# Kernel optimization log

Hardware: AMD Instinct MI355X
Metric: run time of the kernel (lower is better)

Reference implementation:

```python
import jax, jax.numpy as jnp
import numpy as np

D_MODEL = 1024
NUM_HEADS = 16
HEAD_DIM = D_MODEL // NUM_HEADS
B, S = 4, 2048


def setup_inputs() -> dict:
    key = jax.random.key(0)
    ks = jax.random.split(key, 12)
    s = 1.0 / np.sqrt(D_MODEL)
    return {
        "inputs_q": jax.random.normal(ks[0], (B, S, D_MODEL), jnp.float32),
        "inputs_k": jax.random.normal(ks[1], (B, S, D_MODEL), jnp.float32),
        "inputs_v": jax.random.normal(ks[2], (B, S, D_MODEL), jnp.float32),
        "Wq": jax.random.normal(ks[3], (D_MODEL, D_MODEL), jnp.float32) * s,
        "bq": jax.random.normal(ks[4], (D_MODEL,), jnp.float32) * 0.01,
        "Wk": jax.random.normal(ks[5], (D_MODEL, D_MODEL), jnp.float32) * s,
        "bk": jax.random.normal(ks[6], (D_MODEL,), jnp.float32) * 0.01,
        "Wv": jax.random.normal(ks[7], (D_MODEL, D_MODEL), jnp.float32) * s,
        "bv": jax.random.normal(ks[8], (D_MODEL,), jnp.float32) * 0.01,
        "Wo": jax.random.normal(ks[9], (D_MODEL, D_MODEL), jnp.float32) * s,
        "bo": jax.random.normal(ks[10], (D_MODEL,), jnp.float32) * 0.01,
    }


def reference(inputs_q, inputs_k, inputs_v, Wq, bq, Wk, bk, Wv, bv, Wo, bo):
    b, s, _ = inputs_q.shape
    # linear projections
    q = inputs_q @ Wq + bq  # [b, s, d_model]
    k = inputs_k @ Wk + bk
    v = inputs_v @ Wv + bv
    # split heads: bsd -> bhsd
    q = q.reshape(b, s, NUM_HEADS, HEAD_DIM).transpose(0, 2, 1, 3)
    k = k.reshape(b, s, NUM_HEADS, HEAD_DIM).transpose(0, 2, 1, 3)
    v = v.reshape(b, s, NUM_HEADS, HEAD_DIM).transpose(0, 2, 1, 3)
    scale = 1.0 / jnp.sqrt(jnp.asarray(HEAD_DIM, q.dtype))
    scores = jnp.einsum('bhqd,bhkd->bhqk', q, k) * scale  # [b,h,s,s]
    # causal mask: position q attends to k <= q
    causal = jnp.tril(jnp.ones((s, s), dtype=bool))
    scores = jnp.where(causal[None, None], scores, jnp.asarray(-jnp.inf, scores.dtype))
    attn = jax.nn.softmax(scores, axis=-1)
    ctx = jnp.einsum('bhqk,bhkd->bhqd', attn, v)  # [b,h,s,hd]
    ctx = ctx.transpose(0, 2, 1, 3).reshape(b, s, D_MODEL)
    return ctx @ Wo + bo
```

## Files before the change

### kernel.cpp

```cpp
#include <hip/hip_runtime.h>
#include <math.h>
#include <type_traits>

typedef __bf16 bf16;
typedef __attribute__((ext_vector_type(8))) __bf16 bf16x8;
typedef __attribute__((ext_vector_type(4))) float f32x4;

#define SEQ 2048
#define DM 1024
#define NH 16
#define HD 64
#define BATCH 4

#define NEG_BIG (-1e30f)
#define SCALE_L2E 0.18033688011f

__device__ inline bf16x8 cvt_f32x8(const float* p) {
  f32x4 x0 = *(const f32x4*)p;
  f32x4 x1 = *(const f32x4*)(p + 4);
  bf16x8 r;
  r[0] = (bf16)x0[0]; r[1] = (bf16)x0[1]; r[2] = (bf16)x0[2]; r[3] = (bf16)x0[3];
  r[4] = (bf16)x1[0]; r[5] = (bf16)x1[1]; r[6] = (bf16)x1[2]; r[7] = (bf16)x1[3];
  return r;
}

__device__ inline void async_copy16(const bf16* g, bf16* l) {
  __builtin_amdgcn_global_load_lds(
      (const __attribute__((address_space(1))) unsigned int*)g,
      (__attribute__((address_space(3))) unsigned int*)l, 16, 0, 0);
}

__global__ __launch_bounds__(256) void cvt_kernel(const float* __restrict__ src,
                                                  bf16* __restrict__ dst) {
  size_t i = ((size_t)blockIdx.x * 256 + threadIdx.x) * 8;
  *(bf16x8*)(dst + i) = cvt_f32x8(src + i);
}

__global__ __launch_bounds__(256) void transpose_w_kernel(
    const float* __restrict__ Wq, const float* __restrict__ Wk,
    const float* __restrict__ Wv, const float* __restrict__ Wo,
    bf16* __restrict__ Tq, bf16* __restrict__ Tk,
    bf16* __restrict__ Tv, bf16* __restrict__ To) {
  __shared__ bf16 tile[64 * 66];
  int z = blockIdx.z;
  const float* src = (z == 0) ? Wq : (z == 1) ? Wk : (z == 2) ? Wv : Wo;
  bf16* dst = (z == 0) ? Tq : (z == 1) ? Tk : (z == 2) ? Tv : To;
  int n0 = blockIdx.x * 64, k0 = blockIdx.y * 64;
  int t = threadIdx.x;
  int c = t & 63, rr = t >> 6;
#pragma unroll
  for (int i = 0; i < 16; i++) {
    int k = i * 4 + rr;
    tile[k * 66 + c] = (bf16)src[(size_t)(k0 + k) * DM + n0 + c];
  }
  __syncthreads();
#pragma unroll
  for (int i = 0; i < 16; i++) {
    int n = i * 4 + rr;
    dst[(size_t)(n0 + n) * DM + k0 + c] = tile[c * 66 + n];
  }
}

__global__ __launch_bounds__(256) void transpose_v_kernel(
    const bf16* __restrict__ Vc, bf16* __restrict__ Vt) {
  __shared__ bf16 tile[64 * 66];
  int s0 = blockIdx.x * 64;
  int bh = blockIdx.y;
  int t = threadIdx.x;
  int c = t & 63, rr = t >> 6;
  const bf16* src = Vc + (size_t)bh * SEQ * HD;
  bf16* dst = Vt + (size_t)bh * HD * SEQ;
#pragma unroll
  for (int i = 0; i < 16; i++) {
    int s = i * 4 + rr;
    tile[s * 66 + c] = src[(size_t)(s0 + s) * HD + c];
  }
  __syncthreads();
#pragma unroll
  for (int i = 0; i < 16; i++) {
    int d = i * 4 + rr;
    dst[(size_t)d * SEQ + s0 + c] = tile[c * 66 + d];
  }
}

template <typename CT, int MODE>
__global__ __launch_bounds__(256) void gemm_bias_kernel(
    const bf16* __restrict__ A, const bf16* __restrict__ Bt,
    const float* __restrict__ bias, CT* __restrict__ C) {
  __shared__ bf16 As[128 * 32];
  __shared__ bf16 Bs[128 * 32];
  int m0 = blockIdx.x * 128, n0 = blockIdx.y * 128;
  int t = threadIdx.x;
  int wave = t >> 6, lane = t & 63, lr = lane & 15, lq = lane >> 4;
  int wm = (wave & 1) * 64, wn = (wave >> 1) * 64;

  f32x4 acc[4][4];
#pragma unroll
  for (int i = 0; i < 4; i++)
#pragma unroll
    for (int j = 0; j < 4; j++) acc[i][j] = (f32x4){0.f, 0.f, 0.f, 0.f};

  int srow = wave * 32 + (lane >> 2);
  int skc = lane & 3;
  const bf16* gA0 = A + (size_t)(m0 + srow) * DM + skc * 8;
  const bf16* gA1 = gA0 + (size_t)16 * DM;
  const bf16* gB0 = Bt + (size_t)(n0 + srow) * DM + skc * 8;
  const bf16* gB1 = gB0 + (size_t)16 * DM;
  bf16* lA0 = &As[(wave * 128) * 8];
  bf16* lA1 = &As[(wave * 128 + 64) * 8];
  bf16* lB0 = &Bs[(wave * 128) * 8];
  bf16* lB1 = &Bs[(wave * 128 + 64) * 8];

  for (int k0 = 0; k0 < DM; k0 += 32) {
    async_copy16(gA0, lA0);
    async_copy16(gA1, lA1);
    async_copy16(gB0, lB0);
    async_copy16(gB1, lB1);
    gA0 += 32; gA1 += 32; gB0 += 32; gB1 += 32;
    __syncthreads();

    bf16x8 af[4], bfr[4];
#pragma unroll
    for (int i = 0; i < 4; i++)
      af[i] = *(const bf16x8*)&As[(wm + i * 16 + lr) * 32 + lq * 8];
#pragma unroll
    for (int j = 0; j < 4; j++)
      bfr[j] = *(const bf16x8*)&Bs[(wn + j * 16 + lr) * 32 + lq * 8];
#pragma unroll
    for (int i = 0; i < 4; i++)
#pragma unroll
      for (int j = 0; j < 4; j++)
        acc[i][j] = __builtin_amdgcn_mfma_f32_16x16x32_bf16(af[i], bfr[j],
                                                            acc[i][j], 0, 0, 0);
    __syncthreads();
  }

#pragma unroll
  for (int j = 0; j < 4; j++) {
    int col = n0 + wn + j * 16 + lr;
    float bv = bias[col];
#pragma unroll
    for (int i = 0; i < 4; i++) {
      int row0 = m0 + wm + i * 16 + lq * 4;
#pragma unroll
      for (int r = 0; r < 4; r++) {
        int row = row0 + r;
        float v = acc[i][j][r] + bv;
        if constexpr (MODE == 0) {
          C[(size_t)row * DM + col] = (CT)v;
        } else {
          int b = row >> 11, s = row & 2047, h = col >> 6, d = col & 63;
          C[((size_t)(b * NH + h) * SEQ + s) * HD + d] = (CT)v;
        }
      }
    }
  }
}

__global__ __launch_bounds__(256, 2) void attention_kernel(
    const bf16* __restrict__ Qc, const bf16* __restrict__ Kc,
    const bf16* __restrict__ Vt, bf16* __restrict__ ctx) {
  int h = blockIdx.y, b = blockIdx.z;
  int t = threadIdx.x, wave = t >> 6, lane = t & 63, lr = lane & 15,
      lq = lane >> 4;
  int p = blockIdx.x * 4 + wave;

  const bf16* Qb = Qc + (size_t)(b * NH + h) * SEQ * HD;
  const bf16* Kb = Kc + (size_t)(b * NH + h) * SEQ * HD;
  const bf16* Vb = Vt + (size_t)(b * NH + h) * HD * SEQ;
  bf16* Cb = ctx + (size_t)b * SEQ * DM + h * HD;

#pragma unroll 1
  for (int pass = 0; pass < 2; pass++) {
    int tq = pass ? (63 - p) : p;
    int q0 = tq * 32;

    bf16x8 qf[2][2];
#pragma unroll
    for (int qi = 0; qi < 2; qi++)
#pragma unroll
      for (int ks = 0; ks < 2; ks++)
        qf[qi][ks] = *(const bf16x8*)&Qb[(size_t)(q0 + qi * 16 + lr) * HD +
                                         ks * 32 + lq * 8];

    f32x4 o[2][4];
    float m_st[2], l_st[2];
#pragma unroll
    for (int mi = 0; mi < 2; mi++) {
#pragma unroll
      for (int dj = 0; dj < 4; dj++) o[mi][dj] = (f32x4){0.f, 0.f, 0.f, 0.f};
      m_st[mi] = NEG_BIG;
      l_st[mi] = 0.f;
    }

    int kv_end = q0 + 32;
#pragma unroll 1
    for (int kv0 = 0; kv0 < kv_end; kv0 += 64) {
      bf16x8 kf[4][2];
#pragma unroll
      for (int kvt = 0; kvt < 4; kvt++)
#pragma unroll
        for (int ks = 0; ks < 2; ks++)
          kf[kvt][ks] = *(const bf16x8*)&Kb[(size_t)(kv0 + kvt * 16 + lr) * HD +
                                            ks * 32 + lq * 8];
      bf16x8 vf[4][2];
#pragma unroll
      for (int dj = 0; dj < 4; dj++)
#pragma unroll
        for (int ks2 = 0; ks2 < 2; ks2++)
          vf[dj][ks2] = *(const bf16x8*)&Vb[(size_t)(dj * 16 + lr) * SEQ + kv0 +
                                            ks2 * 32 + lq * 8];

      f32x4 s[4][2];
#pragma unroll
      for (int kvt = 0; kvt < 4; kvt++)
#pragma unroll
        for (int qi = 0; qi < 2; qi++) {
          f32x4 acc = (f32x4){0.f, 0.f, 0.f, 0.f};
          acc = __builtin_amdgcn_mfma_f32_16x16x32_bf16(kf[kvt][0], qf[qi][0],
                                                        acc, 0, 0, 0);
          acc = __builtin_amdgcn_mfma_f32_16x16x32_bf16(kf[kvt][1], qf[qi][1],
                                                        acc, 0, 0, 0);
          s[kvt][qi] = acc;
        }

      if (kv0 + 63 > q0) {
#pragma unroll
        for (int kvt = 0; kvt < 4; kvt++)
#pragma unroll
          for (int qi = 0; qi < 2; qi++)
#pragma unroll
            for (int r = 0; r < 4; r++) {
              int kv_g = kv0 + kvt * 16 + lq * 4 + r;
              int q_g = q0 + qi * 16 + lr;
              float v = s[kvt][qi][r] * SCALE_L2E;
              s[kvt][qi][r] = (kv_g > q_g) ? NEG_BIG : v;
            }
      } else {
#pragma unroll
        for (int kvt = 0; kvt < 4; kvt++)
#pragma unroll
          for (int qi = 0; qi < 2; qi++)
#pragma unroll
            for (int r = 0; r < 4; r++) s[kvt][qi][r] *= SCALE_L2E;
      }

      float alpha[2];
#pragma unroll
      for (int qi = 0; qi < 2; qi++) {
        float mx = s[0][qi][0];
#pragma unroll
        for (int kvt = 0; kvt < 4; kvt++)
#pragma unroll
          for (int r = 0; r < 4; r++) mx = fmaxf(mx, s[kvt][qi][r]);
        mx = fmaxf(mx, __shfl_xor(mx, 16));
        mx = fmaxf(mx, __shfl_xor(mx, 32));
        float mnew = fmaxf(m_st[qi], mx);
        alpha[qi] = exp2f(m_st[qi] - mnew);
        m_st[qi] = mnew;
        float rs = 0.f;
#pragma unroll
        for (int kvt = 0; kvt < 4; kvt++)
#pragma unroll
          for (int r = 0; r < 4; r++) {
            float pv = exp2f(s[kvt][qi][r] - mnew);
            s[kvt][qi][r] = pv;
            rs += pv;
          }
        rs += __shfl_xor(rs, 16);
        rs += __shfl_xor(rs, 32);
        l_st[qi] = l_st[qi] * alpha[qi] + rs;
      }

      float aT[2][4];
#pragma unroll
      for (int mi = 0; mi < 2; mi++)
#pragma unroll
        for (int r = 0; r < 4; r++) aT[mi][r] = __shfl(alpha[mi], lq * 4 + r);
#pragma unroll
      for (int mi = 0; mi < 2; mi++)
#pragma unroll
        for (int dj = 0; dj < 4; dj++)
#pragma unroll
          for (int r = 0; r < 4; r++) o[mi][dj][r] *= aT[mi][r];

      int src_base = (lq & 1) * 32 + lr;
      bool hi = (lq >> 1) != 0;
#pragma unroll
      for (int ks2 = 0; ks2 < 2; ks2++) {
        bf16x8 pf[2];
#pragma unroll
        for (int mi = 0; mi < 2; mi++) {
#pragma unroll
          for (int j = 0; j < 8; j++) {
            int src = src_base + (j >> 2) * 16;
            float v0 = __shfl(s[2 * ks2][mi][j & 3], src);
            float v1 = __shfl(s[2 * ks2 + 1][mi][j & 3], src);
            pf[mi][j] = (bf16)(hi ? v1 : v0);
          }
        }
#pragma unroll
        for (int dj = 0; dj < 4; dj++) {
          o[0][dj] = __builtin_amdgcn_mfma_f32_16x16x32_bf16(pf[0], vf[dj][ks2],
                                                             o[0][dj], 0, 0, 0);
          o[1][dj] = __builtin_amdgcn_mfma_f32_16x16x32_bf16(pf[1], vf[dj][ks2],
                                                             o[1][dj], 0, 0, 0);
        }
      }
    }

    float lT[2][4];
#pragma unroll
    for (int mi = 0; mi < 2; mi++)
#pragma unroll
      for (int r = 0; r < 4; r++)
        lT[mi][r] = 1.f / __shfl(l_st[mi], lq * 4 + r);
#pragma unroll
    for (int mi = 0; mi < 2; mi++)
#pragma unroll
      for (int r = 0; r < 4; r++) {
        int row = q0 + mi * 16 + lq * 4 + r;
#pragma unroll
        for (int dj = 0; dj < 4; dj++)
          Cb[(size_t)row * DM + dj * 16 + lr] = (bf16)(o[mi][dj][r] * lT[mi][r]);
      }
  }
}

extern "C" void kernel_launch(void* const* d_in, const int* in_sizes, int n_in,
                              void* d_out, int out_size, void* d_ws,
                              size_t ws_size, hipStream_t stream) {
  const float* iq = (const float*)d_in[0];
  const float* ik = (const float*)d_in[1];
  const float* iv = (const float*)d_in[2];
  const float* Wq = (const float*)d_in[3];
  const float* bq = (const float*)d_in[4];
  const float* Wk = (const float*)d_in[5];
  const float* bk = (const float*)d_in[6];
  const float* Wv = (const float*)d_in[7];
  const float* bv = (const float*)d_in[8];
  const float* Wo = (const float*)d_in[9];
  const float* bo = (const float*)d_in[10];

  char* ws = (char*)d_ws;
  const size_t MB = 1024 * 1024;
  bf16* Tq = (bf16*)(ws + 0 * MB);
  bf16* Tk = (bf16*)(ws + 2 * MB);
  bf16* Tv = (bf16*)(ws + 4 * MB);
  bf16* To = (bf16*)(ws + 6 * MB);
  bf16* Qc = (bf16*)(ws + 8 * MB);
  bf16* Kc = (bf16*)(ws + 24 * MB);
  bf16* Vc = (bf16*)(ws + 40 * MB);
  bf16* X = (bf16*)d_out;
  bf16* Vtp = (bf16*)d_out;
  bf16* Cx = Vc;

  transpose_w_kernel<<<dim3(16, 16, 4), 256, 0, stream>>>(Wq, Wk, Wv, Wo, Tq,
                                                          Tk, Tv, To);
  cvt_kernel<<<dim3(4096), 256, 0, stream>>>(iq, X);
  gemm_bias_kernel<bf16, 1><<<dim3(64, 8), 256, 0, stream>>>(X, Tq, bq, Qc);
  cvt_kernel<<<dim3(4096), 256, 0, stream>>>(ik, X);
  gemm_bias_kernel<bf16, 1><<<dim3(64, 8), 256, 0, stream>>>(X, Tk, bk, Kc);
  cvt_kernel<<<dim3(4096), 256, 0, stream>>>(iv, X);
  gemm_bias_kernel<bf16, 1><<<dim3(64, 8), 256, 0, stream>>>(X, Tv, bv, Vc);
  transpose_v_kernel<<<dim3(32, 64), 256, 0, stream>>>(Vc, Vtp);
  attention_kernel<<<dim3(8, 16, 4), 256, 0, stream>>>(Qc, Kc, Vtp, Cx);
  gemm_bias_kernel<float, 0><<<dim3(64, 8), 256, 0, stream>>>(Cx, To, bo,
                                                              (float*)d_out);
}
```

Measured before the change: 402.7 us.

## Split attention work into one query tile per wave and pack P before shuffling

Each wave now handles a single 32-row query tile instead of two balanced passes. The grid doubles and blocks pair early and late tiles across waves so per-block causal work stays balanced. Launch bounds rise to 4 blocks per CU for more occupancy. Probabilities are packed to bf16 pairs with v_cvt_pk_bf16_f32 before the cross-lane shuffle, halving the shuffle count. Higher occupancy may pressure registers, and within-wave imbalance grows because each wave's tile length now differs.

```diff
diff --git a/kernel.cpp b/kernel.cpp
--- a/kernel.cpp
+++ b/kernel.cpp
@@ -157,174 +157,188 @@
   }
 }
 
-__global__ __launch_bounds__(256, 2) void attention_kernel(
+__global__ __launch_bounds__(256, 4) void attention_kernel(
     const bf16* __restrict__ Qc, const bf16* __restrict__ Kc,
     const bf16* __restrict__ Vt, bf16* __restrict__ ctx) {
   int h = blockIdx.y, b = blockIdx.z;
   int t = threadIdx.x, wave = t >> 6, lane = t & 63, lr = lane & 15,
       lq = lane >> 4;
-  int p = blockIdx.x * 4 + wave;
+
+  int a = blockIdx.x * 2;
+  int w4 = (wave + blockIdx.x) & 3;
+  int tq = (w4 == 0) ? a : (w4 == 1) ? (63 - a) : (w4 == 2) ? (a + 1) : (62 - a);
+  int q0 = tq * 32;
 
   const bf16* Qb = Qc + (size_t)(b * NH + h) * SEQ * HD;
   const bf16* Kb = Kc + (size_t)(b * NH + h) * SEQ * HD;
   const bf16* Vb = Vt + (size_t)(b * NH + h) * HD * SEQ;
   bf16* Cb = ctx + (size_t)b * SEQ * DM + h * HD;
 
+  bf16x8 qf[2][2];
+#pragma unroll
+  for (int qi = 0; qi < 2; qi++)
+#pragma unroll
+    for (int ks = 0; ks < 2; ks++)
+      qf[qi][ks] = *(const bf16x8*)&Qb[(size_t)(q0 + qi * 16 + lr) * HD +
+                                       ks * 32 + lq * 8];
+
+  f32x4 o[2][4];
+  float m_st[2], l_st[2];
+#pragma unroll
+  for (int mi = 0; mi < 2; mi++) {
+#pragma unroll
+    for (int dj = 0; dj < 4; dj++) o[mi][dj] = (f32x4){0.f, 0.f, 0.f, 0.f};
+    m_st[mi] = NEG_BIG;
+    l_st[mi] = 0.f;
+  }
+
+  int kv_end = q0 + 32;
 #pragma unroll 1
-  for (int pass = 0; pass < 2; pass++) {
-    int tq = pass ? (63 - p) : p;
-    int q0 = tq * 32;
-
-    bf16x8 qf[2][2];
-#pragma unroll
-    for (int qi = 0; qi < 2; qi++)
+  for (int kv0 = 0; kv0 < kv_end; kv0 += 64) {
+    bf16x8 kf[4][2];
+#pragma unroll
+    for (int kvt = 0; kvt < 4; kvt++)
 #pragma unroll
       for (int ks = 0; ks < 2; ks++)
-        qf[qi][ks] = *(const bf16x8*)&Qb[(size_t)(q0 + qi * 16 + lr) * HD +
-                                         ks * 32 + lq * 8];
-
-    f32x4 o[2][4];
-    float m_st[2], l_st[2];
-#pragma unroll
-    for (int mi = 0; mi < 2; mi++) {
-#pragma unroll
-      for (int dj = 0; dj < 4; dj++) o[mi][dj] = (f32x4){0.f, 0.f, 0.f, 0.f};
-      m_st[mi] = NEG_BIG;
-      l_st[mi] = 0.f;
-    }
-
-    int kv_end = q0 + 32;
-#pragma unroll 1
-    for (int kv0 = 0; kv0 < kv_end; kv0 += 64) {
-      bf16x8 kf[4][2];
+        kf[kvt][ks] = *(const bf16x8*)&Kb[(size_t)(kv0 + kvt * 16 + lr) * HD +
+                                          ks * 32 + lq * 8];
+    bf16x8 vf[4][2];
+#pragma unroll
+    for (int dj = 0; dj < 4; dj++)
+#pragma unroll
+      for (int ks2 = 0; ks2 < 2; ks2++)
+        vf[dj][ks2] = *(const bf16x8*)&Vb[(size_t)(dj * 16 + lr) * SEQ + kv0 +
+                                          ks2 * 32 + lq * 8];
+
+    f32x4 s[4][2];
+#pragma unroll
+    for (int kvt = 0; kvt < 4; kvt++)
+#pragma unroll
+      for (int qi = 0; qi < 2; qi++) {
+        f32x4 acc = (f32x4){0.f, 0.f, 0.f, 0.f};
+        acc = __builtin_amdgcn_mfma_f32_16x16x32_bf16(kf[kvt][0], qf[qi][0],
+                                                      acc, 0, 0, 0);
+        acc = __builtin_amdgcn_mfma_f32_16x16x32_bf16(kf[kvt][1], qf[qi][1],
+                                                      acc, 0, 0, 0);
+        s[kvt][qi] = acc;
+      }
+
+    if (kv0 + 63 > q0) {
 #pragma unroll
       for (int kvt = 0; kvt < 4; kvt++)
 #pragma unroll
-        for (int ks = 0; ks < 2; ks++)
-          kf[kvt][ks] = *(const bf16x8*)&Kb[(size_t)(kv0 + kvt * 16 + lr) * HD +
-                                            ks * 32 + lq * 8];
-      bf16x8 vf[4][2];
+        for (int qi = 0; qi < 2; qi++)
+#pragma unroll
+          for (int r = 0; r < 4; r++) {
+            int kv_g = kv0 + kvt * 16 + lq * 4 + r;
+            int q_g = q0 + qi * 16 + lr;
+            float v = s[kvt][qi][r] * SCALE_L2E;
+            s[kvt][qi][r] = (kv_g > q_g) ? NEG_BIG : v;
+          }
+    } else {
+#pragma unroll
+      for (int kvt = 0; kvt < 4; kvt++)
+#pragma unroll
+        for (int qi = 0; qi < 2; qi++)
+#pragma unroll
+          for (int r = 0; r < 4; r++) s[kvt][qi][r] *= SCALE_L2E;
+    }
+
+    float alpha[2];
+#pragma unroll
+    for (int qi = 0; qi < 2; qi++) {
+      float mx = s[0][qi][0];
+#pragma unroll
+      for (int kvt = 0; kvt < 4; kvt++)
+#pragma unroll
+        for (int r = 0; r < 4; r++) mx = fmaxf(mx, s[kvt][qi][r]);
+      mx = fmaxf(mx, __shfl_xor(mx, 16));
+      mx = fmaxf(mx, __shfl_xor(mx, 32));
+      float mnew = fmaxf(m_st[qi], mx);
+      alpha[qi] = exp2f(m_st[qi] - mnew);
+      m_st[qi] = mnew;
+      float rs = 0.f;
+#pragma unroll
+      for (int kvt = 0; kvt < 4; kvt++)
+#pragma unroll
+        for (int r = 0; r < 4; r++) {
+          float pv = exp2f(s[kvt][qi][r] - mnew);
+          s[kvt][qi][r] = pv;
+          rs += pv;
+        }
+      rs += __shfl_xor(rs, 16);
+      rs += __shfl_xor(rs, 32);
+      l_st[qi] = l_st[qi] * alpha[qi] + rs;
+    }
+
+    float aT[2][4];
+#pragma unroll
+    for (int mi = 0; mi < 2; mi++)
+#pragma unroll
+      for (int r = 0; r < 4; r++) aT[mi][r] = __shfl(alpha[mi], lq * 4 + r);
+#pragma unroll
+    for (int mi = 0; mi < 2; mi++)
 #pragma unroll
       for (int dj = 0; dj < 4; dj++)
 #pragma unroll
-        for (int ks2 = 0; ks2 < 2; ks2++)
-          vf[dj][ks2] = *(const bf16x8*)&Vb[(size_t)(dj * 16 + lr) * SEQ + kv0 +
-                                            ks2 * 32 + lq * 8];
-
-      f32x4 s[4][2];
-#pragma unroll
-      for (int kvt = 0; kvt < 4; kvt++)
-#pragma unroll
-        for (int qi = 0; qi < 2; qi++) {
-          f32x4 acc = (f32x4){0.f, 0.f, 0.f, 0.f};
-          acc = __builtin_amdgcn_mfma_f32_16x16x32_bf16(kf[kvt][0], qf[qi][0],
-                                                        acc, 0, 0, 0);
-          acc = __builtin_amdgcn_mfma_f32_16x16x32_bf16(kf[kvt][1], qf[qi][1],
-                                                        acc, 0, 0, 0);
-          s[kvt][qi] = acc;
+        for (int r = 0; r < 4; r++) o[mi][dj][r] *= aT[mi][r];
+
+    int src_base = (lq & 1) * 32 + lr;
+    bool hi = (lq >> 1) != 0;
+#pragma unroll
+    for (int ks2 = 0; ks2 < 2; ks2++) {
+      unsigned int pk0[2][2], pk1[2][2];
+#pragma unroll
+      for (int mi = 0; mi < 2; mi++)
+#pragma unroll
+        for (int w = 0; w < 2; w++) {
+          unsigned int r0, r1;
+          asm("v_cvt_pk_bf16_f32 %0, %1, %2"
+              : "=v"(r0)
+              : "v"(s[2 * ks2][mi][2 * w]), "v"(s[2 * ks2][mi][2 * w + 1]));
+          asm("v_cvt_pk_bf16_f32 %0, %1, %2"
+              : "=v"(r1)
+              : "v"(s[2 * ks2 + 1][mi][2 * w]),
+                "v"(s[2 * ks2 + 1][mi][2 * w + 1]));
+          pk0[mi][w] = r0;
+          pk1[mi][w] = r1;
         }
-
-      if (kv0 + 63 > q0) {
-#pragma unroll
-        for (int kvt = 0; kvt < 4; kvt++)
-#pragma unroll
-          for (int qi = 0; qi < 2; qi++)
-#pragma unroll
-            for (int r = 0; r < 4; r++) {
-              int kv_g = kv0 + kvt * 16 + lq * 4 + r;
-              int q_g = q0 + qi * 16 + lr;
-              float v = s[kvt][qi][r] * SCALE_L2E;
-              s[kvt][qi][r] = (kv_g > q_g) ? NEG_BIG : v;
-            }
-      } else {
-#pragma unroll
-        for (int kvt = 0; kvt < 4; kvt++)
-#pragma unroll
-          for (int qi = 0; qi < 2; qi++)
-#pragma unroll
-            for (int r = 0; r < 4; r++) s[kvt][qi][r] *= SCALE_L2E;
-      }
-
-      float alpha[2];
-#pragma unroll
-      for (int qi = 0; qi < 2; qi++) {
-        float mx = s[0][qi][0];
-#pragma unroll
-        for (int kvt = 0; kvt < 4; kvt++)
-#pragma unroll
-          for (int r = 0; r < 4; r++) mx = fmaxf(mx, s[kvt][qi][r]);
-        mx = fmaxf(mx, __shfl_xor(mx, 16));
-        mx = fmaxf(mx, __shfl_xor(mx, 32));
-        float mnew = fmaxf(m_st[qi], mx);
-        alpha[qi] = exp2f(m_st[qi] - mnew);
-        m_st[qi] = mnew;
-        float rs = 0.f;
-#pragma unroll
-        for (int kvt = 0; kvt < 4; kvt++)
-#pragma unroll
-          for (int r = 0; r < 4; r++) {
-            float pv = exp2f(s[kvt][qi][r] - mnew);
-            s[kvt][qi][r] = pv;
-            rs += pv;
-          }
-        rs += __shfl_xor(rs, 16);
-        rs += __shfl_xor(rs, 32);
-        l_st[qi] = l_st[qi] * alpha[qi] + rs;
-      }
-
-      float aT[2][4];
-#pragma unroll
-      for (int mi = 0; mi < 2; mi++)
-#pragma unroll
-        for (int r = 0; r < 4; r++) aT[mi][r] = __shfl(alpha[mi], lq * 4 + r);
-#pragma unroll
-      for (int mi = 0; mi < 2; mi++)
-#pragma unroll
-        for (int dj = 0; dj < 4; dj++)
-#pragma unroll
-          for (int r = 0; r < 4; r++) o[mi][dj][r] *= aT[mi][r];
-
-      int src_base = (lq & 1) * 32 + lr;
-      bool hi = (lq >> 1) != 0;
-#pragma unroll
-      for (int ks2 = 0; ks2 < 2; ks2++) {
-        bf16x8 pf[2];
-#pragma unroll
-        for (int mi = 0; mi < 2; mi++) {
-#pragma unroll
-          for (int j = 0; j < 8; j++) {
-            int src = src_base + (j >> 2) * 16;
-            float v0 = __shfl(s[2 * ks2][mi][j & 3], src);
-            float v1 = __shfl(s[2 * ks2 + 1][mi][j & 3], src);
-            pf[mi][j] = (bf16)(hi ? v1 : v0);
-          }
-        }
-#pragma unroll
-        for (int dj = 0; dj < 4; dj++) {
-          o[0][dj] = __builtin_amdgcn_mfma_f32_16x16x32_bf16(pf[0], vf[dj][ks2],
-                                                             o[0][dj], 0, 0, 0);
-          o[1][dj] = __builtin_amdgcn_mfma_f32_16x16x32_bf16(pf[1], vf[dj][ks2],
-                                                             o[1][dj], 0, 0, 0);
+      bf16x8 pf[2];
+#pragma unroll
+      for (int mi = 0; mi < 2; mi++) {
+#pragma unroll
+        for (int w = 0; w < 4; w++) {
+          int src = src_base + (w >> 1) * 16;
+          unsigned int a0 = (unsigned int)__shfl((int)pk0[mi][w & 1], src);
+          unsigned int a1 = (unsigned int)__shfl((int)pk1[mi][w & 1], src);
+          ((unsigned int*)&pf[mi])[w] = hi ? a1 : a0;
         }
       }
-    }
-
-    float lT[2][4];
-#pragma unroll
-    for (int mi = 0; mi < 2; mi++)
-#pragma unroll
-      for (int r = 0; r < 4; r++)
-        lT[mi][r] = 1.f / __shfl(l_st[mi], lq * 4 + r);
-#pragma unroll
-    for (int mi = 0; mi < 2; mi++)
-#pragma unroll
-      for (int r = 0; r < 4; r++) {
-        int row = q0 + mi * 16 + lq * 4 + r;
-#pragma unroll
-        for (int dj = 0; dj < 4; dj++)
-          Cb[(size_t)row * DM + dj * 16 + lr] = (bf16)(o[mi][dj][r] * lT[mi][r]);
+#pragma unroll
+      for (int dj = 0; dj < 4; dj++) {
+        o[0][dj] = __builtin_amdgcn_mfma_f32_16x16x32_bf16(pf[0], vf[dj][ks2],
+                                                           o[0][dj], 0, 0, 0);
+        o[1][dj] = __builtin_amdgcn_mfma_f32_16x16x32_bf16(pf[1], vf[dj][ks2],
+                                                           o[1][dj], 0, 0, 0);
       }
-  }
+    }
+  }
+
+  float lT[2][4];
+#pragma unroll
+  for (int mi = 0; mi < 2; mi++)
+#pragma unroll
+    for (int r = 0; r < 4; r++)
+      lT[mi][r] = 1.f / __shfl(l_st[mi], lq * 4 + r);
+#pragma unroll
+  for (int mi = 0; mi < 2; mi++)
+#pragma unroll
+    for (int r = 0; r < 4; r++) {
+      int row = q0 + mi * 16 + lq * 4 + r;
+#pragma unroll
+      for (int dj = 0; dj < 4; dj++)
+        Cb[(size_t)row * DM + dj * 16 + lr] = (bf16)(o[mi][dj][r] * lT[mi][r]);
+    }
 }
 
 extern "C" void kernel_launch(void* const* d_in, const int* in_sizes, int n_in,
@@ -364,7 +378,7 @@
   cvt_kernel<<<dim3(4096), 256, 0, stream>>>(iv, X);
   gemm_bias_kernel<bf16, 1><<<dim3(64, 8), 256, 0, stream>>>(X, Tv, bv, Vc);
   transpose_v_kernel<<<dim3(32, 64), 256, 0, stream>>>(Vc, Vtp);
-  attention_kernel<<<dim3(8, 16, 4), 256, 0, stream>>>(Qc, Kc, Vtp, Cx);
+  attention_kernel<<<dim3(16, 16, 4), 256, 0, stream>>>(Qc, Kc, Vtp, Cx);
   gemm_bias_kernel<float, 0><<<dim3(64, 8), 256, 0, stream>>>(Cx, To, bo,
                                                               (float*)d_out);
 }
```

Result: slower. 536.3 us (+33.2%).

## Switch attention kernel to 32x32x16 MFMA with transposed accumulator layout

Applied to the files above, without the earlier changes.

Rewrites the attention inner loop to use 32x32x16 bf16 MFMAs instead of 16x16x32. Scores are computed as K·Q^T, so each lane owns one query row. That removes the per-row alpha and l broadcast shuffles and cuts the P-fragment repacking to a few packed-bf16 xor shuffles. Output is written as packed bf16 pairs. The cost is larger per-lane accumulator tiles, which raise register pressure, and a new lane-mapping scheme that must be exactly right.

```diff
diff --git a/kernel.cpp b/kernel.cpp
--- a/kernel.cpp
+++ b/kernel.cpp
@@ -5,6 +5,7 @@
 typedef __bf16 bf16;
 typedef __attribute__((ext_vector_type(8))) __bf16 bf16x8;
 typedef __attribute__((ext_vector_type(4))) float f32x4;
+typedef __attribute__((ext_vector_type(16))) float f32x16;
 
 #define SEQ 2048
 #define DM 1024
@@ -161,8 +162,8 @@
     const bf16* __restrict__ Qc, const bf16* __restrict__ Kc,
     const bf16* __restrict__ Vt, bf16* __restrict__ ctx) {
   int h = blockIdx.y, b = blockIdx.z;
-  int t = threadIdx.x, wave = t >> 6, lane = t & 63, lr = lane & 15,
-      lq = lane >> 4;
+  int t = threadIdx.x, wave = t >> 6, lane = t & 63;
+  int l31 = lane & 31, hh = lane >> 5;
   int p = blockIdx.x * 4 + wave;
 
   const bf16* Qb = Qc + (size_t)(b * NH + h) * SEQ * HD;
@@ -175,154 +176,147 @@
     int tq = pass ? (63 - p) : p;
     int q0 = tq * 32;
 
-    bf16x8 qf[2][2];
-#pragma unroll
-    for (int qi = 0; qi < 2; qi++)
-#pragma unroll
-      for (int ks = 0; ks < 2; ks++)
-        qf[qi][ks] = *(const bf16x8*)&Qb[(size_t)(q0 + qi * 16 + lr) * HD +
-                                         ks * 32 + lq * 8];
-
-    f32x4 o[2][4];
-    float m_st[2], l_st[2];
-#pragma unroll
-    for (int mi = 0; mi < 2; mi++) {
-#pragma unroll
-      for (int dj = 0; dj < 4; dj++) o[mi][dj] = (f32x4){0.f, 0.f, 0.f, 0.f};
-      m_st[mi] = NEG_BIG;
-      l_st[mi] = 0.f;
+    bf16x8 qf[4];
+#pragma unroll
+    for (int st = 0; st < 4; st++)
+      qf[st] = *(const bf16x8*)&Qb[(size_t)(q0 + l31) * HD + st * 16 + hh * 8];
+
+    f32x16 o[2];
+#pragma unroll
+    for (int dt = 0; dt < 2; dt++)
+#pragma unroll
+      for (int r = 0; r < 16; r++) o[dt][r] = 0.f;
+    float m_st = NEG_BIG, l_st = 0.f;
+
+    int nch = (tq >> 1) + 1;
+#pragma unroll 1
+    for (int c = 0; c < nch; c++) {
+      int kv0 = c * 64;
+      bf16x8 kf[2][4];
+#pragma unroll
+      for (int kt = 0; kt < 2; kt++)
+#pragma unroll
+        for (int st = 0; st < 4; st++)
+          kf[kt][st] = *(const bf16x8*)&Kb[(size_t)(kv0 + kt * 32 + l31) * HD +
+                                           st * 16 + hh * 8];
+      bf16x8 vf[2][4];
+#pragma unroll
+      for (int dt = 0; dt < 2; dt++)
+#pragma unroll
+        for (int ks = 0; ks < 4; ks++)
+          vf[dt][ks] = *(const bf16x8*)&Vb[(size_t)(dt * 32 + l31) * SEQ + kv0 +
+                                           ks * 16 + hh * 8];
+
+      f32x16 s[2];
+#pragma unroll
+      for (int kt = 0; kt < 2; kt++) {
+        f32x16 acc;
+#pragma unroll
+        for (int r = 0; r < 16; r++) acc[r] = 0.f;
+#pragma unroll
+        for (int st = 0; st < 4; st++)
+          acc = __builtin_amdgcn_mfma_f32_32x32x16_bf16(kf[kt][st], qf[st],
+                                                        acc, 0, 0, 0);
+        s[kt] = acc;
+      }
+
+      bool diag = (c == nch - 1);
+      if (diag) {
+        int q_g = q0 + l31;
+#pragma unroll
+        for (int kt = 0; kt < 2; kt++)
+#pragma unroll
+          for (int r = 0; r < 16; r++) {
+            int key = kv0 + kt * 32 + (r & 3) + 8 * (r >> 2) + 4 * hh;
+            float v = s[kt][r] * SCALE_L2E;
+            s[kt][r] = (key > q_g) ? NEG_BIG : v;
+          }
+      } else {
+#pragma unroll
+        for (int kt = 0; kt < 2; kt++)
+#pragma unroll
+          for (int r = 0; r < 16; r++) s[kt][r] *= SCALE_L2E;
+      }
+
+      float mx = s[0][0];
+#pragma unroll
+      for (int r = 1; r < 16; r++) mx = fmaxf(mx, s[0][r]);
+#pragma unroll
+      for (int r = 0; r < 16; r++) mx = fmaxf(mx, s[1][r]);
+      mx = fmaxf(mx, __shfl_xor(mx, 32));
+      float mnew = fmaxf(m_st, mx);
+      float alpha = exp2f(m_st - mnew);
+      m_st = mnew;
+      float rs = 0.f;
+#pragma unroll
+      for (int kt = 0; kt < 2; kt++)
+#pragma unroll
+        for (int r = 0; r < 16; r++) {
+          float pv = exp2f(s[kt][r] - mnew);
+          s[kt][r] = pv;
+          rs += pv;
+        }
+      rs += __shfl_xor(rs, 32);
+      l_st = l_st * alpha + rs;
+#pragma unroll
+      for (int dt = 0; dt < 2; dt++)
+#pragma unroll
+        for (int r = 0; r < 16; r++) o[dt][r] *= alpha;
+
+      unsigned int W[2][8];
+#pragma unroll
+      for (int kt = 0; kt < 2; kt++)
+#pragma unroll
+        for (int w = 0; w < 8; w++) {
+          unsigned int u;
+          asm("v_cvt_pk_bf16_f32 %0, %1, %2"
+              : "=v"(u)
+              : "v"(s[kt][2 * w]), "v"(s[kt][2 * w + 1]));
+          W[kt][w] = u;
+        }
+      bf16x8 pf[4];
+#pragma unroll
+      for (int kt = 0; kt < 2; kt++) {
+        unsigned int x1 = hh ? W[kt][0] : W[kt][2];
+        unsigned int x2 = hh ? W[kt][1] : W[kt][3];
+        unsigned int x3 = hh ? W[kt][4] : W[kt][6];
+        unsigned int x4 = hh ? W[kt][5] : W[kt][7];
+        unsigned int y1 = (unsigned int)__shfl_xor((int)x1, 32);
+        unsigned int y2 = (unsigned int)__shfl_xor((int)x2, 32);
+        unsigned int y3 = (unsigned int)__shfl_xor((int)x3, 32);
+        unsigned int y4 = (unsigned int)__shfl_xor((int)x4, 32);
+        unsigned int* f0 = (unsigned int*)&pf[2 * kt];
+        unsigned int* f1 = (unsigned int*)&pf[2 * kt + 1];
+        f0[0] = hh ? y1 : W[kt][0];
+        f0[1] = hh ? y2 : W[kt][1];
+        f0[2] = hh ? W[kt][2] : y1;
+        f0[3] = hh ? W[kt][3] : y2;
+        f1[0] = hh ? y3 : W[kt][4];
+        f1[1] = hh ? y4 : W[kt][5];
+        f1[2] = hh ? W[kt][6] : y3;
+        f1[3] = hh ? W[kt][7] : y4;
+      }
+
+#pragma unroll
+      for (int dt = 0; dt < 2; dt++)
+#pragma unroll
+        for (int ks = 0; ks < 4; ks++)
+          o[dt] = __builtin_amdgcn_mfma_f32_32x32x16_bf16(vf[dt][ks], pf[ks],
+                                                          o[dt], 0, 0, 0);
     }
 
-    int kv_end = q0 + 32;
-#pragma unroll 1
-    for (int kv0 = 0; kv0 < kv_end; kv0 += 64) {
-      bf16x8 kf[4][2];
-#pragma unroll
-      for (int kvt = 0; kvt < 4; kvt++)
-#pragma unroll
-        for (int ks = 0; ks < 2; ks++)
-          kf[kvt][ks] = *(const bf16x8*)&Kb[(size_t)(kv0 + kvt * 16 + lr) * HD +
-                                            ks * 32 + lq * 8];
-      bf16x8 vf[4][2];
-#pragma unroll
-      for (int dj = 0; dj < 4; dj++)
-#pragma unroll
-        for (int ks2 = 0; ks2 < 2; ks2++)
-          vf[dj][ks2] = *(const bf16x8*)&Vb[(size_t)(dj * 16 + lr) * SEQ + kv0 +
-                                            ks2 * 32 + lq * 8];
-
-      f32x4 s[4][2];
-#pragma unroll
-      for (int kvt = 0; kvt < 4; kvt++)
-#pragma unroll
-        for (int qi = 0; qi < 2; qi++) {
-          f32x4 acc = (f32x4){0.f, 0.f, 0.f, 0.f};
-          acc = __builtin_amdgcn_mfma_f32_16x16x32_bf16(kf[kvt][0], qf[qi][0],
-                                                        acc, 0, 0, 0);
-          acc = __builtin_amdgcn_mfma_f32_16x16x32_bf16(kf[kvt][1], qf[qi][1],
-                                                        acc, 0, 0, 0);
-          s[kvt][qi] = acc;
-        }
-
-      if (kv0 + 63 > q0) {
-#pragma unroll
-        for (int kvt = 0; kvt < 4; kvt++)
-#pragma unroll
-          for (int qi = 0; qi < 2; qi++)
-#pragma unroll
-            for (int r = 0; r < 4; r++) {
-              int kv_g = kv0 + kvt * 16 + lq * 4 + r;
-              int q_g = q0 + qi * 16 + lr;
-              float v = s[kvt][qi][r] * SCALE_L2E;
-              s[kvt][qi][r] = (kv_g > q_g) ? NEG_BIG : v;
-            }
-      } else {
-#pragma unroll
-        for (int kvt = 0; kvt < 4; kvt++)
-#pragma unroll
-          for (int qi = 0; qi < 2; qi++)
-#pragma unroll
-            for (int r = 0; r < 4; r++) s[kvt][qi][r] *= SCALE_L2E;
-      }
-
-      float alpha[2];
-#pragma unroll
-      for (int qi = 0; qi < 2; qi++) {
-        float mx = s[0][qi][0];
-#pragma unroll
-        for (int kvt = 0; kvt < 4; kvt++)
-#pragma unroll
-          for (int r = 0; r < 4; r++) mx = fmaxf(mx, s[kvt][qi][r]);
-        mx = fmaxf(mx, __shfl_xor(mx, 16));
-        mx = fmaxf(mx, __shfl_xor(mx, 32));
-        float mnew = fmaxf(m_st[qi], mx);
-        alpha[qi] = exp2f(m_st[qi] - mnew);
-        m_st[qi] = mnew;
-        float rs = 0.f;
-#pragma unroll
-        for (int kvt = 0; kvt < 4; kvt++)
-#pragma unroll
-          for (int r = 0; r < 4; r++) {
-            float pv = exp2f(s[kvt][qi][r] - mnew);
-            s[kvt][qi][r] = pv;
-            rs += pv;
-          }
-        rs += __shfl_xor(rs, 16);
-        rs += __shfl_xor(rs, 32);
-        l_st[qi] = l_st[qi] * alpha[qi] + rs;
-      }
-
-      float aT[2][4];
-#pragma unroll
-      for (int mi = 0; mi < 2; mi++)
-#pragma unroll
-        for (int r = 0; r < 4; r++) aT[mi][r] = __shfl(alpha[mi], lq * 4 + r);
-#pragma unroll
-      for (int mi = 0; mi < 2; mi++)
-#pragma unroll
-        for (int dj = 0; dj < 4; dj++)
-#pragma unroll
-          for (int r = 0; r < 4; r++) o[mi][dj][r] *= aT[mi][r];
-
-      int src_base = (lq & 1) * 32 + lr;
-      bool hi = (lq >> 1) != 0;
-#pragma unroll
-      for (int ks2 = 0; ks2 < 2; ks2++) {
-        bf16x8 pf[2];
-#pragma unroll
-        for (int mi = 0; mi < 2; mi++) {
-#pragma unroll
-          for (int j = 0; j < 8; j++) {
-            int src = src_base + (j >> 2) * 16;
-            float v0 = __shfl(s[2 * ks2][mi][j & 3], src);
-            float v1 = __shfl(s[2 * ks2 + 1][mi][j & 3], src);
-            pf[mi][j] = (bf16)(hi ? v1 : v0);
-          }
-        }
-#pragma unroll
-        for (int dj = 0; dj < 4; dj++) {
-          o[0][dj] = __builtin_amdgcn_mfma_f32_16x16x32_bf16(pf[0], vf[dj][ks2],
-                                                             o[0][dj], 0, 0, 0);
-          o[1][dj] = __builtin_amdgcn_mfma_f32_16x16x32_bf16(pf[1], vf[dj][ks2],
-                                                             o[1][dj], 0, 0, 0);
-        }
-      }
-    }
-
-    float lT[2][4];
-#pragma unroll
-    for (int mi = 0; mi < 2; mi++)
-#pragma unroll
-      for (int r = 0; r < 4; r++)
-        lT[mi][r] = 1.f / __shfl(l_st[mi], lq * 4 + r);
-#pragma unroll
-    for (int mi = 0; mi < 2; mi++)
-#pragma unroll
-      for (int r = 0; r < 4; r++) {
-        int row = q0 + mi * 16 + lq * 4 + r;
-#pragma unroll
-        for (int dj = 0; dj < 4; dj++)
-          Cb[(size_t)row * DM + dj * 16 + lr] = (bf16)(o[mi][dj][r] * lT[mi][r]);
+    float inv = 1.f / l_st;
+    int row = q0 + l31;
+#pragma unroll
+    for (int dt = 0; dt < 2; dt++)
+#pragma unroll
+      for (int r = 0; r < 16; r += 2) {
+        float va = o[dt][r] * inv;
+        float vb = o[dt][r + 1] * inv;
+        unsigned int u;
+        asm("v_cvt_pk_bf16_f32 %0, %1, %2" : "=v"(u) : "v"(va), "v"(vb));
+        int d = dt * 32 + (r & 3) + 8 * (r >> 2) + 4 * hh;
+        *(unsigned int*)&Cb[(size_t)row * DM + d] = u;
       }
   }
 }
```

Result: no change. 401.3 us (-0.3%).
